# Kernel tuning notes

Hardware: AMD Instinct MI355X
Metric: run time of the kernel (lower is better)

The kernel has to match this reference:

```python
import jax, jax.numpy as jnp
import numpy as np

E = 512        # audio_embd == video_embd
HID = 640      # hidden_dim
NH = 10        # n_heads
DK = HID // NH # 64
BTNK = 4
NUM_CLASSES = 527
B, L_AUD, L_VID = 4, 1024, 1024


def pos_encoding(L, d):
    pos = jnp.arange(L, dtype=jnp.float32)[:, None]
    div = jnp.exp(jnp.arange(0, d, 2, dtype=jnp.float32) * (-np.log(10000.0) / d))
    pe = jnp.zeros((L, d), dtype=jnp.float32)
    pe = pe.at[:, 0::2].set(jnp.sin(pos * div))
    pe = pe.at[:, 1::2].set(jnp.cos(pos * div))
    return pe


def layernorm(x, g, b, eps=1e-5):
    m = jnp.mean(x, axis=-1, keepdims=True)
    v = jnp.var(x, axis=-1, keepdims=True)
    return (x - m) * jax.lax.rsqrt(v + eps) * g + b


def setup_inputs() -> dict:
    key = jax.random.key(0)
    ks = jax.random.split(key, 16)
    s = 0.02
    return {
        "audio_feat": jax.random.normal(ks[0], (B, L_AUD, E), jnp.float32),
        "video_feat": jax.random.normal(ks[1], (B, L_VID, E), jnp.float32),
        "audio_tok": s * jax.random.normal(ks[2], (1, 1, E), jnp.float32),
        "video_tok": s * jax.random.normal(ks[3], (1, 1, E), jnp.float32),
        "btnk_toks": s * jax.random.normal(ks[4], (1, BTNK, E), jnp.float32),
        "Wk": s * jax.random.normal(ks[5], (E, HID), jnp.float32),
        "bk": jnp.zeros((HID,), jnp.float32),
        "Wq": s * jax.random.normal(ks[6], (E, HID), jnp.float32),
        "bq": jnp.zeros((HID,), jnp.float32),
        "Wv": s * jax.random.normal(ks[7], (E, HID), jnp.float32),
        "bv": jnp.zeros((HID,), jnp.float32),
        "ln_g": jnp.ones((HID,), jnp.float32),
        "ln_b": jnp.zeros((HID,), jnp.float32),
        "Wap": s * jax.random.normal(ks[8], (HID, NUM_CLASSES), jnp.float32),
        "bap": jnp.zeros((NUM_CLASSES,), jnp.float32),
        "Wvp": s * jax.random.normal(ks[9], (HID, NUM_CLASSES), jnp.float32),
        "bvp": jnp.zeros((NUM_CLASSES,), jnp.float32),
    }


def reference(audio_feat, video_feat, audio_tok, video_tok, btnk_toks,
              Wk, bk, Wq, bq, Wv, bv, ln_g, ln_b, Wap, bap, Wvp, bvp):
    b, La = audio_feat.shape[:2]
    Lv = video_feat.shape[1]
    # layout: [audio (La), aud_cls (1), bottleneck (BTNK), video (Lv), vid_cls (1)]
    feats = jnp.concatenate([
        audio_feat,
        jnp.broadcast_to(audio_tok, (b, 1, E)),
        jnp.broadcast_to(btnk_toks, (b, BTNK, E)),
        video_feat,
        jnp.broadcast_to(video_tok, (b, 1, E)),
    ], axis=1)
    L = feats.shape[1]
    feats = feats + pos_encoding(L, E)[None]  # dropout is identity at eval

    k = (feats @ Wk + bk).reshape(b, L, NH, DK)
    q = (feats @ Wq + bq).reshape(b, L, NH, DK)
    v = (feats @ Wv + bv).reshape(b, L, NH, DK)

    # NOTE: original computes einsum(k, q) and softmaxes over the q axis (-2).
    attn = jnp.einsum('bmhd,bnhd->bmnh', k, q) / np.sqrt(DK)
    # _get_btnk_mask(L) writes to rows/cols L+1:L+1+BTNK, which are out of
    # range for an (L, L) mask -> mask is all-False (upstream bug, kept faithful).
    attn = jax.nn.softmax(attn, axis=-2)
    out = jnp.einsum('bmnh,bnhd->bmhd', attn, v).reshape(b, L, HID)

    out = layernorm(out, ln_g, ln_b)
    aud_cls = out[:, 0]                 # indices replicate original exactly
    vid_cls = out[:, La + 1 + BTNK]
    aud_pred = aud_cls @ Wap + bap
    vid_pred = vid_cls @ Wvp + bvp
    return (aud_pred + vid_pred) / 2
```

## Files before the change

### kernel.cpp

```cpp
#include <hip/hip_runtime.h>
#include <cstddef>

#define E_DIM 512
#define HID   640
#define NH    10
#define DK    64
#define LTOT  2054
#define NCLS  527
#define NB    4
#define KC    (-0.0179889460390157f)

__device__ __forceinline__ float wave_reduce_sum_dpp(float x) {
    float t;
    t = __int_as_float(__builtin_amdgcn_update_dpp(0, __float_as_int(x), 0x111, 0xf, 0xf, false)); x += t;
    t = __int_as_float(__builtin_amdgcn_update_dpp(0, __float_as_int(x), 0x112, 0xf, 0xf, false)); x += t;
    t = __int_as_float(__builtin_amdgcn_update_dpp(0, __float_as_int(x), 0x114, 0xf, 0xe, false)); x += t;
    t = __int_as_float(__builtin_amdgcn_update_dpp(0, __float_as_int(x), 0x118, 0xf, 0xc, false)); x += t;
    t = __int_as_float(__builtin_amdgcn_update_dpp(0, __float_as_int(x), 0x142, 0xa, 0xf, false)); x += t;
    t = __int_as_float(__builtin_amdgcn_update_dpp(0, __float_as_int(x), 0x143, 0xc, 0xf, false)); x += t;
    return __int_as_float(__builtin_amdgcn_readlane(__float_as_int(x), 63));
}

__device__ __forceinline__ const float* row_src(int b, int n,
        const float* au, const float* vi, const float* at,
        const float* vt, const float* bt) {
    if (n < 1024) return au + ((size_t)b*1024 + n)*E_DIM;
    if (n == 1024) return at;
    if (n < 1029) return bt + (size_t)(n-1025)*E_DIM;
    if (n < 2053) return vi + ((size_t)b*1024 + (n-1029))*E_DIM;
    return vt;
}

__global__ __launch_bounds__(256) void ba_ku_kernel(
        const float* __restrict__ audio, const float* __restrict__ video,
        const float* __restrict__ Wk, const float* __restrict__ bk,
        const float* __restrict__ Wq, const float* __restrict__ bq,
        float* __restrict__ uws, float* __restrict__ cws) {
    int h = blockIdx.x, bm = blockIdx.y;
    int b = bm >> 1, m = bm & 1;
    int mrow = m ? 1029 : 0;
    const float* src = m ? (video + (size_t)b*1024*E_DIM)
                         : (audio + (size_t)b*1024*E_DIM);
    int t = threadIdx.x;
    __shared__ float frow[E_DIM];
    __shared__ __align__(16) float kl[DK];
    __shared__ float red[4][DK];
    for (int i = t; i < E_DIM; i += 256) {
        float div = expf((float)(i & ~1) * KC);
        float arg = (float)mrow * div;
        float pe  = (i & 1) ? cosf(arg) : sinf(arg);
        frow[i] = src[i] + pe;
    }
    __syncthreads();
    int d = t & 63, es = t >> 6;
    const float* wkcol = Wk + (size_t)(h*DK) + d;
    float part = 0.f;
    #pragma unroll 8
    for (int e = es*128; e < es*128 + 128; ++e)
        part = fmaf(frow[e], wkcol[(size_t)e*HID], part);
    red[es][d] = part;
    __syncthreads();
    if (t < DK)
        kl[t] = bk[h*DK + t] + red[0][t] + red[1][t] + red[2][t] + red[3][t];
    __syncthreads();
    #pragma unroll
    for (int s = 0; s < 2; ++s) {
        int e = s*256 + t;
        const float4* wq4 = (const float4*)(Wq + (size_t)e*HID + h*DK);
        const float4* k4  = (const float4*)kl;
        float acc = 0.f;
        #pragma unroll
        for (int d4 = 0; d4 < 16; ++d4) {
            float4 w = wq4[d4]; float4 kk = k4[d4];
            acc = fmaf(w.x,kk.x, fmaf(w.y,kk.y, fmaf(w.z,kk.z, fmaf(w.w,kk.w, acc))));
        }
        uws[((size_t)bm*NH + h)*E_DIM + e] = acc * 0.125f;
    }
    if (t < 64) {
        float prod = (t < DK) ? bq[h*DK + t] * kl[t] : 0.f;
        float tot = wave_reduce_sum_dpp(prod);
        if (t == 0) cws[bm*NH + h] = tot * 0.125f;
    }
}

__global__ __launch_bounds__(128) void ba_fused_kernel(
        const float* __restrict__ audio, const float* __restrict__ video,
        const float* __restrict__ atok, const float* __restrict__ vtok,
        const float* __restrict__ btnk,
        const float* __restrict__ uws, const float* __restrict__ cws,
        float* __restrict__ wpart, float* __restrict__ mcs,
        float* __restrict__ lcs, int nch, int crw) {
    int b = blockIdx.z, chunk = blockIdx.x, t = threadIdx.x;
    int w = t >> 6, lane = t & 63;
    int pbase = (blockIdx.y*2 + w)*2;
    int eb = lane*8;
    float4 u0[2], u1[2];
    float cadd[2];
    #pragma unroll
    for (int i = 0; i < 2; ++i) {
        const float4* up = (const float4*)(uws + (size_t)(b*20 + pbase + i)*E_DIM + eb);
        u0[i] = up[0]; u1[i] = up[1];
        cadd[i] = cws[b*20 + pbase + i];
    }
    int r0 = chunk*crw;
    float sn[4], cn[4], sd[4], cd[4];
    #pragma unroll
    for (int q = 0; q < 4; ++q) {
        float dv = expf((float)(eb + 2*q) * KC);
        sd[q] = sinf(dv); cd[q] = cosf(dv);
        float a = (float)r0 * dv;
        sn[q] = sinf(a); cn[q] = cosf(a);
    }
    float m[2], l[2], acc[2][8];
    #pragma unroll
    for (int i = 0; i < 2; ++i) {
        m[i] = -1e30f; l[i] = 0.f;
        #pragma unroll
        for (int j = 0; j < 8; ++j) acc[i][j] = 0.f;
    }
    int rend = min(r0 + crw, LTOT);

#define ADV_ROT() { \
    _Pragma("unroll") \
    for (int q = 0; q < 4; ++q) { \
        float s2 = fmaf(sn[q], cd[q],  cn[q]*sd[q]); \
        float c2 = fmaf(cn[q], cd[q], -sn[q]*sd[q]); \
        sn[q] = s2; cn[q] = c2; } }

#define DOT8(res, fp, i) { \
    float a_; \
    a_ = (fp)[0]*u0[i].x; \
    a_ = fmaf((fp)[1], u0[i].y, a_); \
    a_ = fmaf((fp)[2], u0[i].z, a_); \
    a_ = fmaf((fp)[3], u0[i].w, a_); \
    a_ = fmaf((fp)[4], u1[i].x, a_); \
    a_ = fmaf((fp)[5], u1[i].y, a_); \
    a_ = fmaf((fp)[6], u1[i].z, a_); \
    a_ = fmaf((fp)[7], u1[i].w, a_); \
    (res) = a_; }

#define SOFT_UPD(i, sc, fp) { \
    if ((sc) > m[i]) { \
        float scale_ = __expf(m[i] - (sc)); \
        m[i] = (sc); \
        l[i] = fmaf(l[i], scale_, 1.f); \
        _Pragma("unroll") \
        for (int j = 0; j < 8; ++j) acc[i][j] = fmaf(acc[i][j], scale_, (fp)[j]); \
    } else { \
        float wg_ = __expf((sc) - m[i]); \
        l[i] += wg_; \
        _Pragma("unroll") \
        for (int j = 0; j < 8; ++j) acc[i][j] = fmaf(wg_, (fp)[j], acc[i][j]); } }

    int r = r0;
    for (; r + 1 < rend; r += 2) {
        const float* srcA = row_src(b, r,   audio, video, atok, vtok, btnk);
        const float* srcB = row_src(b, r+1, audio, video, atok, vtok, btnk);
        float4 a0 = *(const float4*)(srcA + eb);
        float4 a1 = *(const float4*)(srcA + eb + 4);
        float4 b0 = *(const float4*)(srcB + eb);
        float4 b1 = *(const float4*)(srcB + eb + 4);
        float fpA[8], fpB[8];
        fpA[0]=a0.x+sn[0]; fpA[1]=a0.y+cn[0]; fpA[2]=a0.z+sn[1]; fpA[3]=a0.w+cn[1];
        fpA[4]=a1.x+sn[2]; fpA[5]=a1.y+cn[2]; fpA[6]=a1.z+sn[3]; fpA[7]=a1.w+cn[3];
        ADV_ROT();
        fpB[0]=b0.x+sn[0]; fpB[1]=b0.y+cn[0]; fpB[2]=b0.z+sn[1]; fpB[3]=b0.w+cn[1];
        fpB[4]=b1.x+sn[2]; fpB[5]=b1.y+cn[2]; fpB[6]=b1.z+sn[3]; fpB[7]=b1.w+cn[3];
        ADV_ROT();
        float s0, s1, s2, s3;
        DOT8(s0, fpA, 0); DOT8(s1, fpA, 1);
        DOT8(s2, fpB, 0); DOT8(s3, fpB, 1);
        float scA0 = wave_reduce_sum_dpp(s0) + cadd[0];
        float scA1 = wave_reduce_sum_dpp(s1) + cadd[1];
        float scB0 = wave_reduce_sum_dpp(s2) + cadd[0];
        float scB1 = wave_reduce_sum_dpp(s3) + cadd[1];
        SOFT_UPD(0, scA0, fpA); SOFT_UPD(0, scB0, fpB);
        SOFT_UPD(1, scA1, fpA); SOFT_UPD(1, scB1, fpB);
    }
    if (r < rend) {
        const float* srcA = row_src(b, r, audio, video, atok, vtok, btnk);
        float4 a0 = *(const float4*)(srcA + eb);
        float4 a1 = *(const float4*)(srcA + eb + 4);
        float fpA[8];
        fpA[0]=a0.x+sn[0]; fpA[1]=a0.y+cn[0]; fpA[2]=a0.z+sn[1]; fpA[3]=a0.w+cn[1];
        fpA[4]=a1.x+sn[2]; fpA[5]=a1.y+cn[2]; fpA[6]=a1.z+sn[3]; fpA[7]=a1.w+cn[3];
        float s0, s1;
        DOT8(s0, fpA, 0); DOT8(s1, fpA, 1);
        float scA0 = wave_reduce_sum_dpp(s0) + cadd[0];
        float scA1 = wave_reduce_sum_dpp(s1) + cadd[1];
        SOFT_UPD(0, scA0, fpA);
        SOFT_UPD(1, scA1, fpA);
    }
    #pragma unroll
    for (int i = 0; i < 2; ++i) {
        float* dst = wpart + ((size_t)(b*20 + pbase + i)*nch + chunk)*E_DIM + eb;
        *(float4*)dst       = make_float4(acc[i][0], acc[i][1], acc[i][2], acc[i][3]);
        *(float4*)(dst + 4) = make_float4(acc[i][4], acc[i][5], acc[i][6], acc[i][7]);
    }
    float mv = (lane == 0) ? m[0] : m[1];
    float lv = (lane == 0) ? l[0] : l[1];
    if (lane < 2) {
        size_t ix = (size_t)(b*20 + pbase + lane)*nch + chunk;
        mcs[ix] = mv;
        lcs[ix] = lv;
    }
#undef ADV_ROT
#undef DOT8
#undef SOFT_UPD
}

__global__ __launch_bounds__(1024) void ba_outraw_kernel(
        const float* __restrict__ wpart, const float* __restrict__ mcs,
        const float* __restrict__ lcs,
        const float* __restrict__ Wv, const float* __restrict__ bv,
        float* __restrict__ orow, int nch) {
    int h = blockIdx.x, bm = blockIdx.y, t = threadIdx.x;
    int b = bm >> 1, m = bm & 1, p = m*10 + h;
    __shared__ float ml[128], ll[128], coefs[128];
    __shared__ float Msh, invLsh;
    __shared__ float wh[E_DIM];
    __shared__ float sh[2][E_DIM];
    __shared__ float red[16][64];
    const float* mrow = mcs + (size_t)(b*20 + p)*nch;
    const float* lrow = lcs + (size_t)(b*20 + p)*nch;
    if (t < nch) { ml[t] = mrow[t]; ll[t] = lrow[t]; }
    __syncthreads();
    if (t < 64) {
        float mv = -1e30f;
        for (int c = t; c < nch; c += 64) mv = fmaxf(mv, ml[c]);
        #pragma unroll
        for (int off = 1; off < 64; off <<= 1) mv = fmaxf(mv, __shfl_xor(mv, off, 64));
        if (t == 0) Msh = mv;
    }
    __syncthreads();
    float M = Msh;
    if (t < 64) {
        float lv = 0.f;
        for (int c = t; c < nch; c += 64) lv += ll[c] * __expf(ml[c] - M);
        lv = wave_reduce_sum_dpp(lv);
        if (t == 0) invLsh = 1.0f / lv;
    }
    __syncthreads();
    if (t < nch) coefs[t] = __expf(ml[t] - M) * invLsh;
    __syncthreads();
    int e = t & 511, half = t >> 9;
    const float* basep = wpart + (size_t)(b*20 + p)*nch*E_DIM;
    float acc = 0.f;
    int c0 = half*(nch >> 1), c1 = c0 + (nch >> 1);
    for (int c = c0; c < c1; ++c)
        acc = fmaf(basep[(size_t)c*E_DIM + e], coefs[c], acc);
    sh[half][e] = acc;
    __syncthreads();
    if (t < E_DIM) wh[t] = sh[0][t] + sh[1][t];
    __syncthreads();
    int d = t & 63, es = t >> 6;
    float part = 0.f;
    #pragma unroll 8
    for (int e2 = es*32; e2 < es*32 + 32; ++e2)
        part = fmaf(wh[e2], Wv[(size_t)e2*HID + h*DK + d], part);
    red[es][d] = part;
    __syncthreads();
    if (t < 64) {
        float s = 0.f;
        #pragma unroll
        for (int i = 0; i < 16; ++i) s += red[i][t];
        orow[(size_t)bm*HID + h*DK + t] = bv[h*DK + t] + s;
    }
}

__global__ __launch_bounds__(512) void ba_lnpred_kernel(
        const float* __restrict__ orow,
        const float* __restrict__ g, const float* __restrict__ bb,
        const float* __restrict__ Wap, const float* __restrict__ bap,
        const float* __restrict__ Wvp, const float* __restrict__ bvp,
        float* __restrict__ out) {
    int b = blockIdx.y, t = threadIdx.x;
    const float* A = orow + (size_t)(2*b)*HID;
    const float* V = orow + (size_t)(2*b + 1)*HID;
    __shared__ float lnA[HID], lnV[HID];
    __shared__ float wred[4][8];
    __shared__ float psum[8][2][64];
    float sA = 0.f, qA = 0.f, sV = 0.f, qV = 0.f;
    for (int i = t; i < HID; i += 512) {
        float xa = A[i]; sA += xa; qA = fmaf(xa, xa, qA);
        float xv = V[i]; sV += xv; qV = fmaf(xv, xv, qV);
    }
    sA = wave_reduce_sum_dpp(sA); qA = wave_reduce_sum_dpp(qA);
    sV = wave_reduce_sum_dpp(sV); qV = wave_reduce_sum_dpp(qV);
    int w = t >> 6, lane = t & 63;
    if (lane == 0) { wred[0][w] = sA; wred[1][w] = qA; wred[2][w] = sV; wred[3][w] = qV; }
    __syncthreads();
    float tsA = 0.f, tqA = 0.f, tsV = 0.f, tqV = 0.f;
    #pragma unroll
    for (int i = 0; i < 8; ++i) {
        tsA += wred[0][i]; tqA += wred[1][i]; tsV += wred[2][i]; tqV += wred[3][i];
    }
    float meanA = tsA*(1.0f/HID), varA = tqA*(1.0f/HID) - meanA*meanA;
    float meanV = tsV*(1.0f/HID), varV = tqV*(1.0f/HID) - meanV*meanV;
    float rA = rsqrtf(varA + 1e-5f), rV = rsqrtf(varV + 1e-5f);
    for (int i = t; i < HID; i += 512) {
        float gg = g[i], bbv = bb[i];
        lnA[i] = (A[i] - meanA)*rA*gg + bbv;
        lnV[i] = (V[i] - meanV)*rV*gg + bbv;
    }
    __syncthreads();
    int c = blockIdx.x*64 + lane;
    int cc = (c < NCLS) ? c : (NCLS - 1);
    int j0 = w*80;
    float sa = 0.f, sv = 0.f;
    #pragma unroll 8
    for (int j = j0; j < j0 + 80; ++j) {
        sa = fmaf(lnA[j], Wap[(size_t)j*NCLS + cc], sa);
        sv = fmaf(lnV[j], Wvp[(size_t)j*NCLS + cc], sv);
    }
    psum[w][0][lane] = sa;
    psum[w][1][lane] = sv;
    __syncthreads();
    if (t < 64 && c < NCLS) {
        float ta = 0.f, tv = 0.f;
        #pragma unroll
        for (int i = 0; i < 8; ++i) { ta += psum[i][0][t]; tv += psum[i][1][t]; }
        out[(size_t)b*NCLS + c] = 0.5f*(ta + tv + bap[c] + bvp[c]);
    }
}

extern "C" void kernel_launch(void* const* d_in, const int* in_sizes, int n_in,
                              void* d_out, int out_size, void* d_ws, size_t ws_size,
                              hipStream_t stream) {
    const float* audio = (const float*)d_in[0];
    const float* video = (const float*)d_in[1];
    const float* atok  = (const float*)d_in[2];
    const float* vtok  = (const float*)d_in[3];
    const float* btnk  = (const float*)d_in[4];
    const float* Wk    = (const float*)d_in[5];
    const float* bk    = (const float*)d_in[6];
    const float* Wq    = (const float*)d_in[7];
    const float* bq    = (const float*)d_in[8];
    const float* Wv    = (const float*)d_in[9];
    const float* bv    = (const float*)d_in[10];
    const float* ln_g  = (const float*)d_in[11];
    const float* ln_b  = (const float*)d_in[12];
    const float* Wap   = (const float*)d_in[13];
    const float* bap   = (const float*)d_in[14];
    const float* Wvp   = (const float*)d_in[15];
    const float* bvp   = (const float*)d_in[16];
    float* out = (float*)d_out;
    float* ws  = (float*)d_ws;

    auto need = [](int nch) -> size_t {
        return (size_t)(8*NH*E_DIM) + 80
             + (size_t)NB*nch*20*E_DIM + 2*(size_t)NB*nch*20
             + 8*HID;
    };
    int nch = 40;
    if (ws_size >= need(128)*sizeof(float)) nch = 128;
    else if (ws_size >= need(64)*sizeof(float)) nch = 64;
    int crw = (LTOT + nch - 1) / nch;

    float* uws   = ws;
    float* cws   = uws + 8*NH*E_DIM;
    float* wpart = cws + 80;
    float* mcs   = wpart + (size_t)NB*nch*20*E_DIM;
    float* lcs   = mcs + (size_t)NB*nch*20;
    float* orw   = lcs + (size_t)NB*nch*20;

    ba_ku_kernel<<<dim3(NH, 8), 256, 0, stream>>>(audio, video, Wk, bk, Wq, bq, uws, cws);
    ba_fused_kernel<<<dim3(nch, 5, NB), 128, 0, stream>>>(audio, video, atok, vtok, btnk,
                                                          uws, cws, wpart, mcs, lcs, nch, crw);
    ba_outraw_kernel<<<dim3(NH, 8), 1024, 0, stream>>>(wpart, mcs, lcs, Wv, bv, orw, nch);
    ba_lnpred_kernel<<<dim3(9, NB), 512, 0, stream>>>(orw, ln_g, ln_b,
                                                      Wap, bap, Wvp, bvp, out);
}
```

Before: 164.9 us.

## Replace online softmax with two-pass chunk softmax using compile-time chunk length

Makes the chunk row count a template parameter and swaps the per-row online softmax, which branches and rescales the accumulators, for a two-pass scheme. The first pass computes all scores in registers, then the chunk max and the exponential sums; the second pass reloads the rows, recomputes the positional encodings and accumulates the weighted sums. This removes data-dependent branches and serial rescaling chains but loads each input row twice and raises register pressure from the unrolled score arrays. Chunks that start past the sequence end now write neutral partials.

```diff
diff --git a/kernel.cpp b/kernel.cpp
--- a/kernel.cpp
+++ b/kernel.cpp
@@ -83,17 +83,35 @@
     }
 }
 
+template<int CRW>
 __global__ __launch_bounds__(128) void ba_fused_kernel(
         const float* __restrict__ audio, const float* __restrict__ video,
         const float* __restrict__ atok, const float* __restrict__ vtok,
         const float* __restrict__ btnk,
         const float* __restrict__ uws, const float* __restrict__ cws,
         float* __restrict__ wpart, float* __restrict__ mcs,
-        float* __restrict__ lcs, int nch, int crw) {
+        float* __restrict__ lcs, int nch) {
     int b = blockIdx.z, chunk = blockIdx.x, t = threadIdx.x;
     int w = t >> 6, lane = t & 63;
     int pbase = (blockIdx.y*2 + w)*2;
     int eb = lane*8;
+    int r0 = chunk*CRW;
+
+    if (r0 >= LTOT) {
+        #pragma unroll
+        for (int i = 0; i < 2; ++i) {
+            float* dst = wpart + ((size_t)(b*20 + pbase + i)*nch + chunk)*E_DIM + eb;
+            *(float4*)dst       = make_float4(0.f, 0.f, 0.f, 0.f);
+            *(float4*)(dst + 4) = make_float4(0.f, 0.f, 0.f, 0.f);
+        }
+        if (lane < 2) {
+            size_t ix = (size_t)(b*20 + pbase + lane)*nch + chunk;
+            mcs[ix] = -1e30f;
+            lcs[ix] = 0.f;
+        }
+        return;
+    }
+
     float4 u0[2], u1[2];
     float cadd[2];
     #pragma unroll
@@ -102,30 +120,30 @@
         u0[i] = up[0]; u1[i] = up[1];
         cadd[i] = cws[b*20 + pbase + i];
     }
-    int r0 = chunk*crw;
-    float sn[4], cn[4], sd[4], cd[4];
+    float sn[4], cn[4], sd[4], cd[4], sn0[4], cn0[4];
     #pragma unroll
     for (int q = 0; q < 4; ++q) {
         float dv = expf((float)(eb + 2*q) * KC);
         sd[q] = sinf(dv); cd[q] = cosf(dv);
         float a = (float)r0 * dv;
         sn[q] = sinf(a); cn[q] = cosf(a);
-    }
-    float m[2], l[2], acc[2][8];
-    #pragma unroll
-    for (int i = 0; i < 2; ++i) {
-        m[i] = -1e30f; l[i] = 0.f;
-        #pragma unroll
-        for (int j = 0; j < 8; ++j) acc[i][j] = 0.f;
-    }
-    int rend = min(r0 + crw, LTOT);
+        sn0[q] = sn[q]; cn0[q] = cn[q];
+    }
+    int rend = min(r0 + CRW, LTOT);
 
 #define ADV_ROT() { \
     _Pragma("unroll") \
     for (int q = 0; q < 4; ++q) { \
-        float s2 = fmaf(sn[q], cd[q],  cn[q]*sd[q]); \
-        float c2 = fmaf(cn[q], cd[q], -sn[q]*sd[q]); \
-        sn[q] = s2; cn[q] = c2; } }
+        float s2_ = fmaf(sn[q], cd[q],  cn[q]*sd[q]); \
+        float c2_ = fmaf(cn[q], cd[q], -sn[q]*sd[q]); \
+        sn[q] = s2_; cn[q] = c2_; } }
+
+#define LOAD_FP(fp, rr) { \
+    const float* src_ = row_src(b, rr, audio, video, atok, vtok, btnk); \
+    float4 a0_ = *(const float4*)(src_ + eb); \
+    float4 a1_ = *(const float4*)(src_ + eb + 4); \
+    (fp)[0]=a0_.x+sn[0]; (fp)[1]=a0_.y+cn[0]; (fp)[2]=a0_.z+sn[1]; (fp)[3]=a0_.w+cn[1]; \
+    (fp)[4]=a1_.x+sn[2]; (fp)[5]=a1_.y+cn[2]; (fp)[6]=a1_.z+sn[3]; (fp)[7]=a1_.w+cn[3]; }
 
 #define DOT8(res, fp, i) { \
     float a_; \
@@ -139,57 +157,54 @@
     a_ = fmaf((fp)[7], u1[i].w, a_); \
     (res) = a_; }
 
-#define SOFT_UPD(i, sc, fp) { \
-    if ((sc) > m[i]) { \
-        float scale_ = __expf(m[i] - (sc)); \
-        m[i] = (sc); \
-        l[i] = fmaf(l[i], scale_, 1.f); \
-        _Pragma("unroll") \
-        for (int j = 0; j < 8; ++j) acc[i][j] = fmaf(acc[i][j], scale_, (fp)[j]); \
-    } else { \
-        float wg_ = __expf((sc) - m[i]); \
-        l[i] += wg_; \
-        _Pragma("unroll") \
-        for (int j = 0; j < 8; ++j) acc[i][j] = fmaf(wg_, (fp)[j], acc[i][j]); } }
-
-    int r = r0;
-    for (; r + 1 < rend; r += 2) {
-        const float* srcA = row_src(b, r,   audio, video, atok, vtok, btnk);
-        const float* srcB = row_src(b, r+1, audio, video, atok, vtok, btnk);
-        float4 a0 = *(const float4*)(srcA + eb);
-        float4 a1 = *(const float4*)(srcA + eb + 4);
-        float4 b0 = *(const float4*)(srcB + eb);
-        float4 b1 = *(const float4*)(srcB + eb + 4);
-        float fpA[8], fpB[8];
-        fpA[0]=a0.x+sn[0]; fpA[1]=a0.y+cn[0]; fpA[2]=a0.z+sn[1]; fpA[3]=a0.w+cn[1];
-        fpA[4]=a1.x+sn[2]; fpA[5]=a1.y+cn[2]; fpA[6]=a1.z+sn[3]; fpA[7]=a1.w+cn[3];
+    float s0v[CRW], s1v[CRW];
+    #pragma unroll
+    for (int i = 0; i < CRW; ++i) {
+        int r = r0 + i;
+        bool v = (r < rend);
+        int rr = v ? r : (LTOT - 1);
+        float fp[8];
+        LOAD_FP(fp, rr);
         ADV_ROT();
-        fpB[0]=b0.x+sn[0]; fpB[1]=b0.y+cn[0]; fpB[2]=b0.z+sn[1]; fpB[3]=b0.w+cn[1];
-        fpB[4]=b1.x+sn[2]; fpB[5]=b1.y+cn[2]; fpB[6]=b1.z+sn[3]; fpB[7]=b1.w+cn[3];
+        float d0, d1;
+        DOT8(d0, fp, 0); DOT8(d1, fp, 1);
+        float sc0 = wave_reduce_sum_dpp(d0) + cadd[0];
+        float sc1 = wave_reduce_sum_dpp(d1) + cadd[1];
+        s0v[i] = v ? sc0 : -1e30f;
+        s1v[i] = v ? sc1 : -1e30f;
+    }
+    float M0 = -1e30f, M1 = -1e30f;
+    #pragma unroll
+    for (int i = 0; i < CRW; ++i) {
+        M0 = fmaxf(M0, s0v[i]);
+        M1 = fmaxf(M1, s1v[i]);
+    }
+    float L0 = 0.f, L1 = 0.f;
+    #pragma unroll
+    for (int i = 0; i < CRW; ++i) {
+        s0v[i] = __expf(s0v[i] - M0); L0 += s0v[i];
+        s1v[i] = __expf(s1v[i] - M1); L1 += s1v[i];
+    }
+    #pragma unroll
+    for (int q = 0; q < 4; ++q) { sn[q] = sn0[q]; cn[q] = cn0[q]; }
+    float acc[2][8];
+    #pragma unroll
+    for (int i = 0; i < 2; ++i)
+        #pragma unroll
+        for (int j = 0; j < 8; ++j) acc[i][j] = 0.f;
+    #pragma unroll
+    for (int i = 0; i < CRW; ++i) {
+        int r = r0 + i;
+        int rr = (r < rend) ? r : (LTOT - 1);
+        float fp[8];
+        LOAD_FP(fp, rr);
         ADV_ROT();
-        float s0, s1, s2, s3;
-        DOT8(s0, fpA, 0); DOT8(s1, fpA, 1);
-        DOT8(s2, fpB, 0); DOT8(s3, fpB, 1);
-        float scA0 = wave_reduce_sum_dpp(s0) + cadd[0];
-        float scA1 = wave_reduce_sum_dpp(s1) + cadd[1];
-        float scB0 = wave_reduce_sum_dpp(s2) + cadd[0];
-        float scB1 = wave_reduce_sum_dpp(s3) + cadd[1];
-        SOFT_UPD(0, scA0, fpA); SOFT_UPD(0, scB0, fpB);
-        SOFT_UPD(1, scA1, fpA); SOFT_UPD(1, scB1, fpB);
-    }
-    if (r < rend) {
-        const float* srcA = row_src(b, r, audio, video, atok, vtok, btnk);
-        float4 a0 = *(const float4*)(srcA + eb);
-        float4 a1 = *(const float4*)(srcA + eb + 4);
-        float fpA[8];
-        fpA[0]=a0.x+sn[0]; fpA[1]=a0.y+cn[0]; fpA[2]=a0.z+sn[1]; fpA[3]=a0.w+cn[1];
-        fpA[4]=a1.x+sn[2]; fpA[5]=a1.y+cn[2]; fpA[6]=a1.z+sn[3]; fpA[7]=a1.w+cn[3];
-        float s0, s1;
-        DOT8(s0, fpA, 0); DOT8(s1, fpA, 1);
-        float scA0 = wave_reduce_sum_dpp(s0) + cadd[0];
-        float scA1 = wave_reduce_sum_dpp(s1) + cadd[1];
-        SOFT_UPD(0, scA0, fpA);
-        SOFT_UPD(1, scA1, fpA);
+        float w0 = s0v[i], w1 = s1v[i];
+        #pragma unroll
+        for (int j = 0; j < 8; ++j) {
+            acc[0][j] = fmaf(w0, fp[j], acc[0][j]);
+            acc[1][j] = fmaf(w1, fp[j], acc[1][j]);
+        }
     }
     #pragma unroll
     for (int i = 0; i < 2; ++i) {
@@ -197,16 +212,16 @@
         *(float4*)dst       = make_float4(acc[i][0], acc[i][1], acc[i][2], acc[i][3]);
         *(float4*)(dst + 4) = make_float4(acc[i][4], acc[i][5], acc[i][6], acc[i][7]);
     }
-    float mv = (lane == 0) ? m[0] : m[1];
-    float lv = (lane == 0) ? l[0] : l[1];
+    float mv = (lane == 0) ? M0 : M1;
+    float lv = (lane == 0) ? L0 : L1;
     if (lane < 2) {
         size_t ix = (size_t)(b*20 + pbase + lane)*nch + chunk;
         mcs[ix] = mv;
         lcs[ix] = lv;
     }
 #undef ADV_ROT
+#undef LOAD_FP
 #undef DOT8
-#undef SOFT_UPD
 }
 
 __global__ __launch_bounds__(1024) void ba_outraw_kernel(
@@ -355,7 +370,6 @@
     int nch = 40;
     if (ws_size >= need(128)*sizeof(float)) nch = 128;
     else if (ws_size >= need(64)*sizeof(float)) nch = 64;
-    int crw = (LTOT + nch - 1) / nch;
 
     float* uws   = ws;
     float* cws   = uws + 8*NH*E_DIM;
@@ -365,8 +379,15 @@
     float* orw   = lcs + (size_t)NB*nch*20;
 
     ba_ku_kernel<<<dim3(NH, 8), 256, 0, stream>>>(audio, video, Wk, bk, Wq, bq, uws, cws);
-    ba_fused_kernel<<<dim3(nch, 5, NB), 128, 0, stream>>>(audio, video, atok, vtok, btnk,
-                                                          uws, cws, wpart, mcs, lcs, nch, crw);
+    if (nch == 128)
+        ba_fused_kernel<17><<<dim3(128, 5, NB), 128, 0, stream>>>(
+            audio, video, atok, vtok, btnk, uws, cws, wpart, mcs, lcs, 128);
+    else if (nch == 64)
+        ba_fused_kernel<33><<<dim3(64, 5, NB), 128, 0, stream>>>(
+            audio, video, atok, vtok, btnk, uws, cws, wpart, mcs, lcs, 64);
+    else
+        ba_fused_kernel<52><<<dim3(40, 5, NB), 128, 0, stream>>>(
+            audio, video, atok, vtok, btnk, uws, cws, wpart, mcs, lcs, 40);
     ba_outraw_kernel<<<dim3(NH, 8), 1024, 0, stream>>>(wpart, mcs, lcs, Wv, bv, orw, nch);
     ba_lnpred_kernel<<<dim3(9, NB), 512, 0, stream>>>(orw, ln_g, ln_b,
                                                       Wap, bap, Wvp, bvp, out);
```

Result: slower. 190.2 us (+15.4%).

## Stage feature chunk in LDS and compute all 20 heads per block

Applied to the files above, without the earlier changes.

The fused attention kernel now loads a CRW-row chunk of positional-encoded features into shared memory once per block and serves all 20 (m,h) query vectors from it. Before, five separate blocks each re-read the same rows. Per-row online softmax is replaced by a two-phase scheme: scores go to LDS, then a per-chunk max and exp pass, then a weighted-sum pass. This cuts redundant global reads and the wave reductions per row. In exchange it uses much more LDS per block, computes sin/cos directly per element, and changes the chunk count to 121 or 41, which lowers occupancy and also affects the outraw kernel's split reduction.

```diff
diff --git a/kernel.cpp b/kernel.cpp
--- a/kernel.cpp
+++ b/kernel.cpp
@@ -9,6 +9,7 @@
 #define NCLS  527
 #define NB    4
 #define KC    (-0.0179889460390157f)
+#define FPITCH 516
 
 __device__ __forceinline__ float wave_reduce_sum_dpp(float x) {
     float t;
@@ -19,6 +20,11 @@
     t = __int_as_float(__builtin_amdgcn_update_dpp(0, __float_as_int(x), 0x142, 0xa, 0xf, false)); x += t;
     t = __int_as_float(__builtin_amdgcn_update_dpp(0, __float_as_int(x), 0x143, 0xc, 0xf, false)); x += t;
     return __int_as_float(__builtin_amdgcn_readlane(__float_as_int(x), 63));
+}
+
+__device__ __forceinline__ void fma4(float4& a, const float4& x, const float4& y) {
+    a.x = fmaf(x.x, y.x, a.x); a.y = fmaf(x.y, y.y, a.y);
+    a.z = fmaf(x.z, y.z, a.z); a.w = fmaf(x.w, y.w, a.w);
 }
 
 __device__ __forceinline__ const float* row_src(int b, int n,
@@ -83,130 +89,111 @@
     }
 }
 
-__global__ __launch_bounds__(128) void ba_fused_kernel(
+template<int CRW>
+__global__ __launch_bounds__(256) void ba_fused_kernel(
         const float* __restrict__ audio, const float* __restrict__ video,
         const float* __restrict__ atok, const float* __restrict__ vtok,
         const float* __restrict__ btnk,
         const float* __restrict__ uws, const float* __restrict__ cws,
         float* __restrict__ wpart, float* __restrict__ mcs,
-        float* __restrict__ lcs, int nch, int crw) {
-    int b = blockIdx.z, chunk = blockIdx.x, t = threadIdx.x;
+        float* __restrict__ lcs, int nch) {
+    __shared__ __align__(16) float Fl[CRW*FPITCH];
+    __shared__ __align__(16) float Ul[20*FPITCH];
+    __shared__ float Sl[CRW*20];
+    __shared__ float cadd_l[20];
+    int b = blockIdx.y, chunk = blockIdx.x, t = threadIdx.x;
+    int r0 = chunk*CRW;
+
+    for (int idx = t; idx < CRW*E_DIM; idx += 256) {
+        int r = idx >> 9, e = idx & 511;
+        int n = r0 + r;
+        float val = 0.f;
+        if (n < LTOT) {
+            const float* src = row_src(b, n, audio, video, atok, vtok, btnk);
+            float dv  = expf((float)(e & ~1) * KC);
+            float arg = (float)n * dv;
+            float pe  = (e & 1) ? cosf(arg) : sinf(arg);
+            val = src[e] + pe;
+        }
+        Fl[r*FPITCH + e] = val;
+    }
+    for (int idx = t; idx < 20*E_DIM; idx += 256) {
+        int p = idx >> 9, e = idx & 511;
+        Ul[p*FPITCH + e] = uws[((size_t)(b*20 + p) << 9) + e];
+    }
+    if (t < 20) cadd_l[t] = cws[b*20 + t];
+    __syncthreads();
+
+    for (int pair = t; pair < CRW*10; pair += 256) {
+        int r = pair / 10, pp = pair % 10;
+        int p0 = pp*2, p1 = p0 + 1;
+        const float4* Fr = (const float4*)(Fl + r*FPITCH);
+        const float4* U0 = (const float4*)(Ul + p0*FPITCH);
+        const float4* U1 = (const float4*)(Ul + p1*FPITCH);
+        float4 a00 = make_float4(0,0,0,0), a01 = make_float4(0,0,0,0);
+        float4 a10 = make_float4(0,0,0,0), a11 = make_float4(0,0,0,0);
+        #pragma unroll 4
+        for (int e4 = 0; e4 < 128; e4 += 2) {
+            float4 f0 = Fr[e4], f1 = Fr[e4+1];
+            fma4(a00, f0, U0[e4]);   fma4(a01, f1, U0[e4+1]);
+            fma4(a10, f0, U1[e4]);   fma4(a11, f1, U1[e4+1]);
+        }
+        bool valid = (r0 + r < LTOT);
+        float s0 = (a00.x+a00.y+a00.z+a00.w) + (a01.x+a01.y+a01.z+a01.w) + cadd_l[p0];
+        float s1 = (a10.x+a10.y+a10.z+a10.w) + (a11.x+a11.y+a11.z+a11.w) + cadd_l[p1];
+        Sl[r*20 + p0] = valid ? s0 : -1e30f;
+        Sl[r*20 + p1] = valid ? s1 : -1e30f;
+    }
+    __syncthreads();
+
+    if (t < 20) {
+        float M = -1e30f;
+        #pragma unroll
+        for (int r = 0; r < CRW; ++r) M = fmaxf(M, Sl[r*20 + t]);
+        float L = 0.f;
+        #pragma unroll
+        for (int r = 0; r < CRW; ++r) {
+            float wv = __expf(Sl[r*20 + t] - M);
+            Sl[r*20 + t] = wv;
+            L += wv;
+        }
+        size_t ix = (size_t)(b*20 + t)*nch + chunk;
+        mcs[ix] = M;
+        lcs[ix] = L;
+    }
+    __syncthreads();
+
     int w = t >> 6, lane = t & 63;
-    int pbase = (blockIdx.y*2 + w)*2;
     int eb = lane*8;
-    float4 u0[2], u1[2];
-    float cadd[2];
+    float4 acc0[5], acc1[5];
     #pragma unroll
-    for (int i = 0; i < 2; ++i) {
-        const float4* up = (const float4*)(uws + (size_t)(b*20 + pbase + i)*E_DIM + eb);
-        u0[i] = up[0]; u1[i] = up[1];
-        cadd[i] = cws[b*20 + pbase + i];
-    }
-    int r0 = chunk*crw;
-    float sn[4], cn[4], sd[4], cd[4];
+    for (int i = 0; i < 5; ++i) {
+        acc0[i] = make_float4(0,0,0,0);
+        acc1[i] = make_float4(0,0,0,0);
+    }
+    #pragma unroll 2
+    for (int r = 0; r < CRW; ++r) {
+        const float4* Fr = (const float4*)(Fl + r*FPITCH + eb);
+        float4 f0 = Fr[0], f1 = Fr[1];
+        #pragma unroll
+        for (int i = 0; i < 5; ++i) {
+            float wl = Sl[r*20 + w*5 + i];
+            acc0[i].x = fmaf(wl, f0.x, acc0[i].x);
+            acc0[i].y = fmaf(wl, f0.y, acc0[i].y);
+            acc0[i].z = fmaf(wl, f0.z, acc0[i].z);
+            acc0[i].w = fmaf(wl, f0.w, acc0[i].w);
+            acc1[i].x = fmaf(wl, f1.x, acc1[i].x);
+            acc1[i].y = fmaf(wl, f1.y, acc1[i].y);
+            acc1[i].z = fmaf(wl, f1.z, acc1[i].z);
+            acc1[i].w = fmaf(wl, f1.w, acc1[i].w);
+        }
+    }
     #pragma unroll
-    for (int q = 0; q < 4; ++q) {
-        float dv = expf((float)(eb + 2*q) * KC);
-        sd[q] = sinf(dv); cd[q] = cosf(dv);
-        float a = (float)r0 * dv;
-        sn[q] = sinf(a); cn[q] = cosf(a);
-    }
-    float m[2], l[2], acc[2][8];
-    #pragma unroll
-    for (int i = 0; i < 2; ++i) {
-        m[i] = -1e30f; l[i] = 0.f;
-        #pragma unroll
-        for (int j = 0; j < 8; ++j) acc[i][j] = 0.f;
-    }
-    int rend = min(r0 + crw, LTOT);
-
-#define ADV_ROT() { \
-    _Pragma("unroll") \
-    for (int q = 0; q < 4; ++q) { \
-        float s2 = fmaf(sn[q], cd[q],  cn[q]*sd[q]); \
-        float c2 = fmaf(cn[q], cd[q], -sn[q]*sd[q]); \
-        sn[q] = s2; cn[q] = c2; } }
-
-#define DOT8(res, fp, i) { \
-    float a_; \
-    a_ = (fp)[0]*u0[i].x; \
-    a_ = fmaf((fp)[1], u0[i].y, a_); \
-    a_ = fmaf((fp)[2], u0[i].z, a_); \
-    a_ = fmaf((fp)[3], u0[i].w, a_); \
-    a_ = fmaf((fp)[4], u1[i].x, a_); \
-    a_ = fmaf((fp)[5], u1[i].y, a_); \
-    a_ = fmaf((fp)[6], u1[i].z, a_); \
-    a_ = fmaf((fp)[7], u1[i].w, a_); \
-    (res) = a_; }
-
-#define SOFT_UPD(i, sc, fp) { \
-    if ((sc) > m[i]) { \
-        float scale_ = __expf(m[i] - (sc)); \
-        m[i] = (sc); \
-        l[i] = fmaf(l[i], scale_, 1.f); \
-        _Pragma("unroll") \
-        for (int j = 0; j < 8; ++j) acc[i][j] = fmaf(acc[i][j], scale_, (fp)[j]); \
-    } else { \
-        float wg_ = __expf((sc) - m[i]); \
-        l[i] += wg_; \
-        _Pragma("unroll") \
-        for (int j = 0; j < 8; ++j) acc[i][j] = fmaf(wg_, (fp)[j], acc[i][j]); } }
-
-    int r = r0;
-    for (; r + 1 < rend; r += 2) {
-        const float* srcA = row_src(b, r,   audio, video, atok, vtok, btnk);
-        const float* srcB = row_src(b, r+1, audio, video, atok, vtok, btnk);
-        float4 a0 = *(const float4*)(srcA + eb);
-        float4 a1 = *(const float4*)(srcA + eb + 4);
-        float4 b0 = *(const float4*)(srcB + eb);
-        float4 b1 = *(const float4*)(srcB + eb + 4);
-        float fpA[8], fpB[8];
-        fpA[0]=a0.x+sn[0]; fpA[1]=a0.y+cn[0]; fpA[2]=a0.z+sn[1]; fpA[3]=a0.w+cn[1];
-        fpA[4]=a1.x+sn[2]; fpA[5]=a1.y+cn[2]; fpA[6]=a1.z+sn[3]; fpA[7]=a1.w+cn[3];
-        ADV_ROT();
-        fpB[0]=b0.x+sn[0]; fpB[1]=b0.y+cn[0]; fpB[2]=b0.z+sn[1]; fpB[3]=b0.w+cn[1];
-        fpB[4]=b1.x+sn[2]; fpB[5]=b1.y+cn[2]; fpB[6]=b1.z+sn[3]; fpB[7]=b1.w+cn[3];
-        ADV_ROT();
-        float s0, s1, s2, s3;
-        DOT8(s0, fpA, 0); DOT8(s1, fpA, 1);
-        DOT8(s2, fpB, 0); DOT8(s3, fpB, 1);
-        float scA0 = wave_reduce_sum_dpp(s0) + cadd[0];
-        float scA1 = wave_reduce_sum_dpp(s1) + cadd[1];
-        float scB0 = wave_reduce_sum_dpp(s2) + cadd[0];
-        float scB1 = wave_reduce_sum_dpp(s3) + cadd[1];
-        SOFT_UPD(0, scA0, fpA); SOFT_UPD(0, scB0, fpB);
-        SOFT_UPD(1, scA1, fpA); SOFT_UPD(1, scB1, fpB);
-    }
-    if (r < rend) {
-        const float* srcA = row_src(b, r, audio, video, atok, vtok, btnk);
-        float4 a0 = *(const float4*)(srcA + eb);
-        float4 a1 = *(const float4*)(srcA + eb + 4);
-        float fpA[8];
-        fpA[0]=a0.x+sn[0]; fpA[1]=a0.y+cn[0]; fpA[2]=a0.z+sn[1]; fpA[3]=a0.w+cn[1];
-        fpA[4]=a1.x+sn[2]; fpA[5]=a1.y+cn[2]; fpA[6]=a1.z+sn[3]; fpA[7]=a1.w+cn[3];
-        float s0, s1;
-        DOT8(s0, fpA, 0); DOT8(s1, fpA, 1);
-        float scA0 = wave_reduce_sum_dpp(s0) + cadd[0];
-        float scA1 = wave_reduce_sum_dpp(s1) + cadd[1];
-        SOFT_UPD(0, scA0, fpA);
-        SOFT_UPD(1, scA1, fpA);
-    }
-    #pragma unroll
-    for (int i = 0; i < 2; ++i) {
-        float* dst = wpart + ((size_t)(b*20 + pbase + i)*nch + chunk)*E_DIM + eb;
-        *(float4*)dst       = make_float4(acc[i][0], acc[i][1], acc[i][2], acc[i][3]);
-        *(float4*)(dst + 4) = make_float4(acc[i][4], acc[i][5], acc[i][6], acc[i][7]);
-    }
-    float mv = (lane == 0) ? m[0] : m[1];
-    float lv = (lane == 0) ? l[0] : l[1];
-    if (lane < 2) {
-        size_t ix = (size_t)(b*20 + pbase + lane)*nch + chunk;
-        mcs[ix] = mv;
-        lcs[ix] = lv;
-    }
-#undef ADV_ROT
-#undef DOT8
-#undef SOFT_UPD
+    for (int i = 0; i < 5; ++i) {
+        float* dst = wpart + ((size_t)(b*20 + w*5 + i)*nch + chunk)*E_DIM + eb;
+        *(float4*)dst       = acc0[i];
+        *(float4*)(dst + 4) = acc1[i];
+    }
 }
 
 __global__ __launch_bounds__(1024) void ba_outraw_kernel(
@@ -246,7 +233,8 @@
     int e = t & 511, half = t >> 9;
     const float* basep = wpart + (size_t)(b*20 + p)*nch*E_DIM;
     float acc = 0.f;
-    int c0 = half*(nch >> 1), c1 = c0 + (nch >> 1);
+    int c0 = half ? (nch >> 1) : 0;
+    int c1 = half ? nch : (nch >> 1);
     for (int c = c0; c < c1; ++c)
         acc = fmaf(basep[(size_t)c*E_DIM + e], coefs[c], acc);
     sh[half][e] = acc;
@@ -352,10 +340,7 @@
              + (size_t)NB*nch*20*E_DIM + 2*(size_t)NB*nch*20
              + 8*HID;
     };
-    int nch = 40;
-    if (ws_size >= need(128)*sizeof(float)) nch = 128;
-    else if (ws_size >= need(64)*sizeof(float)) nch = 64;
-    int crw = (LTOT + nch - 1) / nch;
+    int nch = (ws_size >= need(121)*sizeof(float)) ? 121 : 41;
 
     float* uws   = ws;
     float* cws   = uws + 8*NH*E_DIM;
@@ -365,8 +350,12 @@
     float* orw   = lcs + (size_t)NB*nch*20;
 
     ba_ku_kernel<<<dim3(NH, 8), 256, 0, stream>>>(audio, video, Wk, bk, Wq, bq, uws, cws);
-    ba_fused_kernel<<<dim3(nch, 5, NB), 128, 0, stream>>>(audio, video, atok, vtok, btnk,
-                                                          uws, cws, wpart, mcs, lcs, nch, crw);
+    if (nch == 121)
+        ba_fused_kernel<17><<<dim3(121, NB), 256, 0, stream>>>(
+            audio, video, atok, vtok, btnk, uws, cws, wpart, mcs, lcs, 121);
+    else
+        ba_fused_kernel<51><<<dim3(41, NB), 256, 0, stream>>>(
+            audio, video, atok, vtok, btnk, uws, cws, wpart, mcs, lcs, 41);
     ba_outraw_kernel<<<dim3(NH, 8), 1024, 0, stream>>>(wpart, mcs, lcs, Wv, bv, orw, nch);
     ba_lnpred_kernel<<<dim3(9, NB), 512, 0, stream>>>(orw, ln_g, ln_b,
                                                       Wap, bap, Wvp, bvp, out);
```

After: 176.7 us. 1.07x slower.
